# Performance work log

Measured on AMD Instinct MI355X. Metric: run time of the kernel, lower is better.

Reference implementation:

```python
import jax, jax.numpy as jnp
import numpy as np
import math

L, D, H, DH, DFF, V, NB, MAXD = 4, 512, 8, 64, 1024, 32128, 32, 128
B, S = 2, 2048
EPS = 1e-6


def gelu_new(x):
    return 0.5 * x * (1.0 + jnp.tanh(math.sqrt(2.0 / math.pi) * (x + 0.044715 * x ** 3)))


def t5_layernorm(x, w):
    var = jnp.mean(jnp.square(x.astype(jnp.float32)), axis=-1, keepdims=True)
    return w * (x * jax.lax.rsqrt(var + EPS))


def relative_position_bucket(rel_pos, num_buckets=NB, max_distance=MAXD):
    # bidirectional T5 bucketing
    nb = num_buckets // 2
    buckets = (rel_pos > 0).astype(jnp.int32) * nb
    rp = jnp.abs(rel_pos)
    max_exact = nb // 2
    is_small = rp < max_exact
    rp_large = max_exact + (
        jnp.log(jnp.maximum(rp, 1).astype(jnp.float32) / max_exact)
        / math.log(max_distance / max_exact) * (nb - max_exact)
    ).astype(jnp.int32)
    rp_large = jnp.minimum(rp_large, nb - 1)
    return buckets + jnp.where(is_small, rp, rp_large)


def compute_bias(rel_bias_table, q_len, k_len):
    ctx = jnp.arange(q_len)[:, None]
    mem = jnp.arange(k_len)[None, :]
    buckets = relative_position_bucket(mem - ctx)              # [S, S]
    vals = rel_bias_table[buckets]                             # [S, S, H]
    return jnp.transpose(vals, (2, 0, 1))[None]                # [1, H, S, S]


def setup_inputs() -> dict:
    key = jax.random.key(0)
    ks = jax.random.split(key, 12)
    s = 0.02
    return {
        "input_ids": jax.random.randint(ks[0], (B, S), 0, V),
        "embed": jax.random.normal(ks[1], (V, D), jnp.float32) * s,
        "Wq": jax.random.normal(ks[2], (L, D, H * DH), jnp.float32) * s,
        "Wk": jax.random.normal(ks[3], (L, D, H * DH), jnp.float32) * s,
        "Wv": jax.random.normal(ks[4], (L, D, H * DH), jnp.float32) * s,
        "Wo": jax.random.normal(ks[5], (L, H * DH, D), jnp.float32) * s,
        "rel_bias": jax.random.normal(ks[6], (NB, H), jnp.float32) * s,
        "wi0": jax.random.normal(ks[7], (L, D, DFF), jnp.float32) * s,
        "wi1": jax.random.normal(ks[8], (L, D, DFF), jnp.float32) * s,
        "wo_ffn": jax.random.normal(ks[9], (L, DFF, D), jnp.float32) * s,
        "ln0_w": jnp.ones((L, D), jnp.float32),
        "ln1_w": jnp.ones((L, D), jnp.float32),
        "final_ln_w": jnp.ones((D,), jnp.float32),
    }


def encoder_forward(input_ids, embed, Wq, Wk, Wv, Wo, rel_bias, wi0, wi1, wo_ffn, ln0_w, ln1_w, final_ln_w):
    x = embed[input_ids]                                       # [B, S, D]
    pos_bias = compute_bias(rel_bias, S, S)                    # [1, H, S, S], reused across layers
    for i in range(L):
        # --- self-attention (T5: no 1/sqrt(d) scaling) ---
        h = t5_layernorm(x, ln0_w[i])
        q = (h @ Wq[i]).reshape(B, S, H, DH)
        k = (h @ Wk[i]).reshape(B, S, H, DH)
        v = (h @ Wv[i]).reshape(B, S, H, DH)
        scores = jnp.einsum('bqhd,bkhd->bhqk', q, k) + pos_bias
        attn = jax.nn.softmax(scores, axis=-1)
        o = jnp.einsum('bhqk,bkhd->bqhd', attn, v).reshape(B, S, H * DH)
        x = x + o @ Wo[i]
        # --- gated-GELU FFN ---
        h = t5_layernorm(x, ln1_w[i])
        g = gelu_new(h @ wi0[i]) * (h @ wi1[i])
        x = x + g @ wo_ffn[i]
    out = t5_layernorm(x, final_ln_w)
    return out, pos_bias


def reference(input_ids, embed, Wq, Wk, Wv, Wo, rel_bias, wi0, wi1, wo_ffn, ln0_w, ln1_w, final_ln_w):
    return encoder_forward(input_ids, embed, Wq, Wk, Wv, Wo, rel_bias, wi0, wi1, wo_ffn, ln0_w, ln1_w, final_ln_w)
```

## Files before the change

### kernel.cpp

```cpp
#include <hip/hip_runtime.h>

#define NTOK 4096

typedef float f32x4 __attribute__((ext_vector_type(4)));
typedef short s16x8 __attribute__((ext_vector_type(8)));
typedef unsigned short u16x4 __attribute__((ext_vector_type(4)));
typedef unsigned short u16x8 __attribute__((ext_vector_type(8)));

__device__ __forceinline__ unsigned short fbf(float f) {
  unsigned int u = __float_as_uint(f);
  return (unsigned short)((u + 0x7FFFu + ((u >> 16) & 1u)) >> 16);
}
__device__ __forceinline__ float bf2f(unsigned short s) {
  return __uint_as_float(((unsigned int)s) << 16);
}
__device__ __forceinline__ float gelu_new_f(float x) {
  float inner = 0.7978845608028654f * (x + 0.044715f * x * x * x);
  return 0.5f * x * (1.0f + tanhf(inner));
}

__device__ __forceinline__ void gl_lds16(const void* g, void* l) {
  __builtin_amdgcn_global_load_lds(
      (const __attribute__((address_space(1))) unsigned int*)g,
      (__attribute__((address_space(3))) unsigned int*)l, 16, 0, 0);
}

__global__ void embed_kernel(const int* __restrict__ ids, const float* __restrict__ emb,
                             float* __restrict__ x) {
  int tok = blockIdx.x;
  int id = ids[tok];
  int t = threadIdx.x;
  *(float4*)(x + (size_t)tok * 512 + t * 4) = *(const float4*)(emb + (size_t)id * 512 + t * 4);
}

__global__ void build_dbias_kernel(const float* __restrict__ rel_bias, float* __restrict__ dbias) {
  int d = blockIdx.x * 256 + threadIdx.x;
  if (d >= 4096) return;
  int rel = d - 2047;
  int bucket = (rel > 0) ? 16 : 0;
  int rp = rel < 0 ? -rel : rel;
  if (rp < 8) {
    bucket += rp;
  } else {
    float v = logf((float)rp / 8.0f) / logf(16.0f) * 8.0f;
    int rl = 8 + (int)v;
    bucket += (rl < 15) ? rl : 15;
  }
  for (int hh = 0; hh < 8; ++hh)
    dbias[hh * 4096 + d] = rel_bias[bucket * 8 + hh];
}

__global__ void posbias_kernel(const float* __restrict__ dbias, float* __restrict__ out1) {
  size_t g = (size_t)blockIdx.x * 256 + threadIdx.x;
  int k4 = (int)(g & 511) * 4;
  int qq = (int)((g >> 9) & 2047);
  int hh = (int)(g >> 20);
  const float* src = dbias + hh * 4096 + (k4 - qq + 2047);
  *(float4*)(out1 + g * 4) = make_float4(src[0], src[1], src[2], src[3]);
}

__global__ void rmsnorm_bf16_kernel(const float* __restrict__ x, const float* __restrict__ w,
                                    unsigned short* __restrict__ out) {
  int tok = blockIdx.x;
  int t = threadIdx.x;
  float4 v = *(const float4*)(x + (size_t)tok * 512 + t * 4);
  float ss = v.x * v.x + v.y * v.y + v.z * v.z + v.w * v.w;
  for (int m = 1; m < 64; m <<= 1) ss += __shfl_xor(ss, m, 64);
  __shared__ float part[2];
  if ((t & 63) == 0) part[t >> 6] = ss;
  __syncthreads();
  float scale = rsqrtf((part[0] + part[1]) * (1.0f / 512.0f) + 1e-6f);
  float4 wv = *(const float4*)(w + t * 4);
  u16x4 o = {fbf(wv.x * v.x * scale), fbf(wv.y * v.y * scale),
             fbf(wv.z * v.z * scale), fbf(wv.w * v.w * scale)};
  *(u16x4*)(out + (size_t)tok * 512 + t * 4) = o;
}

__global__ void rmsnorm_f32_kernel(const float* __restrict__ x, const float* __restrict__ w,
                                   float* __restrict__ out) {
  int tok = blockIdx.x;
  int t = threadIdx.x;
  float4 v = *(const float4*)(x + (size_t)tok * 512 + t * 4);
  float ss = v.x * v.x + v.y * v.y + v.z * v.z + v.w * v.w;
  for (int m = 1; m < 64; m <<= 1) ss += __shfl_xor(ss, m, 64);
  __shared__ float part[2];
  if ((t & 63) == 0) part[t >> 6] = ss;
  __syncthreads();
  float scale = rsqrtf((part[0] + part[1]) * (1.0f / 512.0f) + 1e-6f);
  float4 wv = *(const float4*)(w + t * 4);
  *(float4*)(out + (size_t)tok * 512 + t * 4) =
      make_float4(wv.x * v.x * scale, wv.y * v.y * scale, wv.z * v.z * scale, wv.w * v.w * scale);
}

__global__ void transw_kernel(const float* S0, const float* S1, const float* S2, const float* S3,
                              unsigned short* D0, unsigned short* D1, unsigned short* D2,
                              unsigned short* D3, int R, int C) {
  __shared__ float tile[32][33];
  int mat = blockIdx.z >> 2, layer = blockIdx.z & 3;
  const float* src = (mat == 0 ? S0 : mat == 1 ? S1 : mat == 2 ? S2 : S3) + (size_t)layer * R * C;
  unsigned short* dst = (mat == 0 ? D0 : mat == 1 ? D1 : mat == 2 ? D2 : D3) + (size_t)layer * R * C;
  int t = threadIdx.x;
  int r0 = blockIdx.y * 32, c0 = blockIdx.x * 32;
  int tr = t >> 3, tc = (t & 7) * 4;
  float4 v = *(const float4*)(src + (size_t)(r0 + tr) * C + c0 + tc);
  tile[tr][tc] = v.x; tile[tr][tc + 1] = v.y; tile[tr][tc + 2] = v.z; tile[tr][tc + 3] = v.w;
  __syncthreads();
  u16x4 o = {fbf(tile[tc + 0][tr]), fbf(tile[tc + 1][tr]),
             fbf(tile[tc + 2][tr]), fbf(tile[tc + 3][tr])};
  *(u16x4*)(dst + (size_t)(c0 + tr) * R + r0 + tc) = o;
}

__global__ __launch_bounds__(256) void gemm64_kernel(
    const unsigned short* __restrict__ A,
    const unsigned short* B0, const unsigned short* B1, const unsigned short* B2,
    void* C0, void* C1, void* C2, const float* __restrict__ Res,
    int M, int N, int K, int m0, int m1, int m2) {
  __shared__ unsigned short As[2][64 * 64];
  __shared__ unsigned short Bs[2][64 * 64];
  const int z = blockIdx.z;
  const unsigned short* B = (z == 0) ? B0 : (z == 1) ? B1 : B2;
  void* Cptr = (z == 0) ? C0 : (z == 1) ? C1 : C2;
  const int mode = (z == 0) ? m0 : (z == 1) ? m1 : m2;
  const int t = threadIdx.x, lane = t & 63, w = t >> 6;
  const int quad = lane >> 4, c = lane & 15;
  const int wr = w >> 1, wc = w & 1;
  const int row0 = blockIdx.y * 64, col0 = blockIdx.x * 64;
  const int ar = t >> 3, aj = t & 7;
  const int asrc8 = (aj ^ (ar & 7)) * 8;
  const unsigned short* Agl = A + (size_t)(row0 + ar) * K + asrc8;
  const unsigned short* Bgl = B + (size_t)(col0 + ar) * K + asrc8;
  f32x4 acc[2][2];
#pragma unroll
  for (int i = 0; i < 2; ++i)
#pragma unroll
    for (int j = 0; j < 2; ++j) { f32x4 zz = {0.f, 0.f, 0.f, 0.f}; acc[i][j] = zz; }

  gl_lds16(Agl, &As[0][w * 512]);
  gl_lds16(Agl + 32 * (size_t)K, &As[0][2048 + w * 512]);
  gl_lds16(Bgl, &Bs[0][w * 512]);
  gl_lds16(Bgl + 32 * (size_t)K, &Bs[0][2048 + w * 512]);
  __syncthreads();

  int p = 0;
  for (int k0 = 0; k0 < K; k0 += 64) {
    if (k0 + 64 < K) {
      gl_lds16(Agl + k0 + 64, &As[p ^ 1][w * 512]);
      gl_lds16(Agl + k0 + 64 + 32 * (size_t)K, &As[p ^ 1][2048 + w * 512]);
      gl_lds16(Bgl + k0 + 64, &Bs[p ^ 1][w * 512]);
      gl_lds16(Bgl + k0 + 64 + 32 * (size_t)K, &Bs[p ^ 1][2048 + w * 512]);
    }
    s16x8 af[2][2], bf[2][2];
#pragma unroll
    for (int rb = 0; rb < 2; ++rb) {
      int r = wr * 32 + rb * 16 + c;
      int n = wc * 32 + rb * 16 + c;
#pragma unroll
      for (int ks = 0; ks < 2; ++ks) {
        af[rb][ks] = *(const s16x8*)&As[p][r * 64 + (((ks * 4 + quad) ^ (r & 7)) << 3)];
        bf[rb][ks] = *(const s16x8*)&Bs[p][n * 64 + (((ks * 4 + quad) ^ (n & 7)) << 3)];
      }
    }
#pragma unroll
    for (int rb = 0; rb < 2; ++rb)
#pragma unroll
      for (int cb = 0; cb < 2; ++cb)
#pragma unroll
        for (int ks = 0; ks < 2; ++ks)
          acc[rb][cb] = __builtin_amdgcn_mfma_f32_16x16x32_bf16(af[rb][ks], bf[cb][ks], acc[rb][cb], 0, 0, 0);
    __syncthreads();
    p ^= 1;
  }

  const int mb = row0 + wr * 32 + quad * 4;
  const int nb = col0 + wc * 32 + c;
  if (mode == 0) {
    unsigned short* Cp = (unsigned short*)Cptr;
#pragma unroll
    for (int rb = 0; rb < 2; ++rb)
#pragma unroll
      for (int cb = 0; cb < 2; ++cb) {
        size_t base = (size_t)(mb + rb * 16) * N + nb + cb * 16;
#pragma unroll
        for (int reg = 0; reg < 4; ++reg) Cp[base + (size_t)reg * N] = fbf(acc[rb][cb][reg]);
      }
  } else if (mode == 1) {
    unsigned short* Cp = (unsigned short*)Cptr;
#pragma unroll
    for (int rb = 0; rb < 2; ++rb)
#pragma unroll
      for (int cb = 0; cb < 2; ++cb) {
        u16x4 pk = {fbf(acc[rb][cb][0]), fbf(acc[rb][cb][1]), fbf(acc[rb][cb][2]), fbf(acc[rb][cb][3])};
        *(u16x4*)&Cp[(size_t)(nb + cb * 16) * M + mb + rb * 16] = pk;
      }
  } else {
    float* Cf = (float*)Cptr;
#pragma unroll
    for (int rb = 0; rb < 2; ++rb)
#pragma unroll
      for (int cb = 0; cb < 2; ++cb)
#pragma unroll
        for (int reg = 0; reg < 4; ++reg) {
          size_t o = (size_t)(mb + rb * 16 + reg) * N + nb + cb * 16;
          Cf[o] = Res[o] + acc[rb][cb][reg];
        }
  }
}

__global__ __launch_bounds__(256) void gemm_ffn_kernel(
    const unsigned short* __restrict__ A, const unsigned short* __restrict__ B0g,
    const unsigned short* __restrict__ B1g, unsigned short* __restrict__ C) {
  __shared__ unsigned short As[2][128 * 64];
  __shared__ unsigned short Bs0[2][64 * 64];
  __shared__ unsigned short Bs1[2][64 * 64];
  const int t = threadIdx.x, lane = t & 63, w = t >> 6;
  const int quad = lane >> 4, c = lane & 15;
  const int wr = w >> 1, wc = w & 1;
  const int row0 = blockIdx.y * 128, col0 = blockIdx.x * 64;
  const int K = 512;
  f32x4 acc0[4][2], acc1[4][2];
#pragma unroll
  for (int i = 0; i < 4; ++i)
#pragma unroll
    for (int j = 0; j < 2; ++j) {
      f32x4 zz = {0.f, 0.f, 0.f, 0.f};
      acc0[i][j] = zz; acc1[i][j] = zz;
    }

  const int ar = t >> 3, aj = t & 7;
  const int asrc8 = (aj ^ (ar & 7)) * 8;
  const unsigned short* Agl = A + (size_t)(row0 + ar) * K + asrc8;
  const unsigned short* B0gl = B0g + (size_t)(col0 + ar) * K + asrc8;
  const unsigned short* B1gl = B1g + (size_t)(col0 + ar) * K + asrc8;

  auto stage = [&](int pp, int kk) {
    gl_lds16(Agl + kk, &As[pp][w * 512]);
    gl_lds16(Agl + kk + 32 * (size_t)K, &As[pp][2048 + w * 512]);
    gl_lds16(Agl + kk + 64 * (size_t)K, &As[pp][4096 + w * 512]);
    gl_lds16(Agl + kk + 96 * (size_t)K, &As[pp][6144 + w * 512]);
    gl_lds16(B0gl + kk, &Bs0[pp][w * 512]);
    gl_lds16(B0gl + kk + 32 * (size_t)K, &Bs0[pp][2048 + w * 512]);
    gl_lds16(B1gl + kk, &Bs1[pp][w * 512]);
    gl_lds16(B1gl + kk + 32 * (size_t)K, &Bs1[pp][2048 + w * 512]);
  };

  stage(0, 0);
  __syncthreads();

  int p = 0;
  for (int k0 = 0; k0 < K; k0 += 64) {
    if (k0 + 64 < K) stage(p ^ 1, k0 + 64);
    s16x8 af[4][2], bf0[2][2], bf1[2][2];
#pragma unroll
    for (int rb = 0; rb < 4; ++rb) {
      int r = wr * 64 + rb * 16 + c;
#pragma unroll
      for (int ks = 0; ks < 2; ++ks)
        af[rb][ks] = *(const s16x8*)&As[p][r * 64 + (((ks * 4 + quad) ^ (r & 7)) << 3)];
    }
#pragma unroll
    for (int cb = 0; cb < 2; ++cb) {
      int n = wc * 32 + cb * 16 + c;
#pragma unroll
      for (int ks = 0; ks < 2; ++ks) {
        bf0[cb][ks] = *(const s16x8*)&Bs0[p][n * 64 + (((ks * 4 + quad) ^ (n & 7)) << 3)];
        bf1[cb][ks] = *(const s16x8*)&Bs1[p][n * 64 + (((ks * 4 + quad) ^ (n & 7)) << 3)];
      }
    }
#pragma unroll
    for (int rb = 0; rb < 4; ++rb)
#pragma unroll
      for (int cb = 0; cb < 2; ++cb)
#pragma unroll
        for (int ks = 0; ks < 2; ++ks) {
          acc0[rb][cb] = __builtin_amdgcn_mfma_f32_16x16x32_bf16(af[rb][ks], bf0[cb][ks], acc0[rb][cb], 0, 0, 0);
          acc1[rb][cb] = __builtin_amdgcn_mfma_f32_16x16x32_bf16(af[rb][ks], bf1[cb][ks], acc1[rb][cb], 0, 0, 0);
        }
    __syncthreads();
    p ^= 1;
  }

  const int mb = row0 + wr * 64 + quad * 4;
  const int nb = col0 + wc * 32 + c;
#pragma unroll
  for (int rb = 0; rb < 4; ++rb)
#pragma unroll
    for (int cb = 0; cb < 2; ++cb) {
      size_t base = (size_t)(mb + rb * 16) * 1024 + nb + cb * 16;
#pragma unroll
      for (int reg = 0; reg < 4; ++reg)
        C[base + (size_t)reg * 1024] = fbf(gelu_new_f(acc0[rb][cb][reg]) * acc1[rb][cb][reg]);
    }
}

__global__ __launch_bounds__(256) void attn_split_kernel(
    const unsigned short* __restrict__ qg, const unsigned short* __restrict__ kg,
    const unsigned short* __restrict__ vtg, const float* __restrict__ dbias,
    unsigned short* __restrict__ Op0, unsigned short* __restrict__ Op1,
    unsigned short* __restrict__ Op2, unsigned short* __restrict__ Op3,
    float* __restrict__ lsum) {
  __shared__ unsigned short Ks[64 * 64];
  __shared__ unsigned short Vs[64 * 64];
  __shared__ unsigned short Ps[4][16 * 64];
  __shared__ float Bb[128];
  const int b = blockIdx.z, hh = blockIdx.y;
  const int q0b = (blockIdx.x & 31) * 64;
  const int split = blockIdx.x >> 5;
  unsigned short* Op = (split == 0) ? Op0 : (split == 1) ? Op1 : (split == 2) ? Op2 : Op3;
  const int t = threadIdx.x, lane = t & 63, w = t >> 6;
  const int quad = lane >> 4, c = lane & 15;
  const int hd = hh * 64;
  s16x8 qf[2];
#pragma unroll
  for (int ks = 0; ks < 2; ++ks)
    qf[ks] = *(const s16x8*)(qg + (size_t)(b * 2048 + q0b + w * 16 + c) * 512 + hd + ks * 32 + quad * 8);
  f32x4 oacc[4];
  float psum[4];
#pragma unroll
  for (int i = 0; i < 4; ++i) {
    f32x4 zz = {0.f, 0.f, 0.f, 0.f};
    oacc[i] = zz; psum[i] = 0.f;
  }
  const int biasbase = hh * 4096 + 2047 - q0b - 63;
  const int rowloc = w * 16 + quad * 4;
  const int srow = t >> 3, sjj = t & 7;
  const unsigned short* kbase = kg + (size_t)(b * 2048) * 512 + hd;
  const unsigned short* vbase = vtg + (size_t)hd * 4096 + b * 2048;

  s16x8 kpre[2], vpre[2];
  float bpre;
  {
    int k0 = split * 8 * 64;
#pragma unroll
    for (int v = 0; v < 2; ++v) {
      int row = srow + 32 * v;
      kpre[v] = *(const s16x8*)(kbase + (size_t)(k0 + row) * 512 + sjj * 8);
      vpre[v] = *(const s16x8*)(vbase + (size_t)row * 4096 + k0 + sjj * 8);
    }
    bpre = dbias[biasbase + k0 + (t & 127)];
  }

  for (int kt = split * 8; kt < split * 8 + 8; ++kt) {
    __syncthreads();
#pragma unroll
    for (int v = 0; v < 2; ++v) {
      int row = srow + 32 * v;
      int ch = (sjj ^ (row & 7)) << 3;
      *(s16x8*)&Ks[row * 64 + ch] = kpre[v];
      *(s16x8*)&Vs[row * 64 + ch] = vpre[v];
    }
    if (t < 128) Bb[t] = bpre;
    __syncthreads();
    {
      int k0n = (kt + 1 < split * 8 + 8) ? (kt + 1) * 64 : kt * 64;
#pragma unroll
      for (int v = 0; v < 2; ++v) {
        int row = srow + 32 * v;
        kpre[v] = *(const s16x8*)(kbase + (size_t)(k0n + row) * 512 + sjj * 8);
        vpre[v] = *(const s16x8*)(vbase + (size_t)row * 4096 + k0n + sjj * 8);
      }
      bpre = dbias[biasbase + k0n + (t & 127)];
    }

    f32x4 s[4];
#pragma unroll
    for (int i = 0; i < 4; ++i) { f32x4 zz = {0.f, 0.f, 0.f, 0.f}; s[i] = zz; }
#pragma unroll
    for (int ks = 0; ks < 2; ++ks)
#pragma unroll
      for (int cb = 0; cb < 4; ++cb) {
        int n = cb * 16 + c;
        s16x8 kf = *(const s16x8*)&Ks[n * 64 + (((ks * 4 + quad) ^ (n & 7)) << 3)];
        s[cb] = __builtin_amdgcn_mfma_f32_16x16x32_bf16(qf[ks], kf, s[cb], 0, 0, 0);
      }
#pragma unroll
    for (int cb = 0; cb < 4; ++cb) {
      int col = cb * 16 + c;
      int chunkbase = (col >> 3);
#pragma unroll
      for (int reg = 0; reg < 4; ++reg) {
        float pp = __expf(s[cb][reg] + Bb[col - rowloc - reg + 63]);
        psum[reg] += pp;
        int rowp = quad * 4 + reg;
        Ps[w][rowp * 64 + ((chunkbase ^ (rowp & 7)) << 3) + (col & 7)] = fbf(pp);
      }
    }
#pragma unroll
    for (int ks = 0; ks < 2; ++ks) {
      s16x8 pf = *(const s16x8*)&Ps[w][c * 64 + (((ks * 4 + quad) ^ (c & 7)) << 3)];
#pragma unroll
      for (int cbo = 0; cbo < 4; ++cbo) {
        int n = cbo * 16 + c;
        s16x8 vf = *(const s16x8*)&Vs[n * 64 + (((ks * 4 + quad) ^ (n & 7)) << 3)];
        oacc[cbo] = __builtin_amdgcn_mfma_f32_16x16x32_bf16(pf, vf, oacc[cbo], 0, 0, 0);
      }
    }
  }
#pragma unroll
  for (int reg = 0; reg < 4; ++reg) {
    float ps = psum[reg];
    ps += __shfl_xor(ps, 1, 64);
    ps += __shfl_xor(ps, 2, 64);
    ps += __shfl_xor(ps, 4, 64);
    ps += __shfl_xor(ps, 8, 64);
    psum[reg] = ps;
  }
  const size_t obase = ((size_t)(b * 8 + hh) * 2048 + q0b + w * 16 + quad * 4);
#pragma unroll
  for (int cbo = 0; cbo < 4; ++cbo)
#pragma unroll
    for (int reg = 0; reg < 4; ++reg)
      Op[(obase + reg) * 64 + cbo * 16 + c] = fbf(oacc[cbo][reg]);
  if (c == 0) {
    const size_t lbase = (size_t)split * 32768 + (size_t)(b * 8 + hh) * 2048 + q0b + w * 16 + quad * 4;
#pragma unroll
    for (int reg = 0; reg < 4; ++reg) lsum[lbase + reg] = psum[reg];
  }
}

__global__ void attn_combine_kernel(const unsigned short* __restrict__ O0,
                                    const unsigned short* __restrict__ O1,
                                    const unsigned short* __restrict__ O2,
                                    const unsigned short* __restrict__ O3,
                                    const float* __restrict__ lsum,
                                    unsigned short* __restrict__ out) {
  int gr = blockIdx.x * 16 + (threadIdx.x >> 4);
  int d4 = (threadIdx.x & 15) * 4;
  float inv = 1.0f / (lsum[gr] + lsum[32768 + gr] + lsum[65536 + gr] + lsum[98304 + gr]);
  u16x4 p0 = *(const u16x4*)(O0 + (size_t)gr * 64 + d4);
  u16x4 p1 = *(const u16x4*)(O1 + (size_t)gr * 64 + d4);
  u16x4 p2 = *(const u16x4*)(O2 + (size_t)gr * 64 + d4);
  u16x4 p3 = *(const u16x4*)(O3 + (size_t)gr * 64 + d4);
  int bidx = gr >> 14, hidx = (gr >> 11) & 7, row = gr & 2047;
  u16x4 o;
#pragma unroll
  for (int u = 0; u < 4; ++u)
    o[u] = fbf((bf2f(p0[u]) + bf2f(p1[u]) + bf2f(p2[u]) + bf2f(p3[u])) * inv);
  *(u16x4*)(out + ((size_t)(bidx * 2048 + row) * 512) + hidx * 64 + d4) = o;
}

extern "C" void kernel_launch(void* const* d_in, const int* in_sizes, int n_in,
                              void* d_out, int out_size, void* d_ws, size_t ws_size,
                              hipStream_t stream) {
  const int*   ids      = (const int*)d_in[0];
  const float* embed    = (const float*)d_in[1];
  const float* Wq       = (const float*)d_in[2];
  const float* Wk       = (const float*)d_in[3];
  const float* Wv       = (const float*)d_in[4];
  const float* Wo       = (const float*)d_in[5];
  const float* rel_bias = (const float*)d_in[6];
  const float* wi0      = (const float*)d_in[7];
  const float* wi1      = (const float*)d_in[8];
  const float* wo_ffn   = (const float*)d_in[9];
  const float* ln0      = (const float*)d_in[10];
  const float* ln1      = (const float*)d_in[11];
  const float* final_ln = (const float*)d_in[12];
  float* out = (float*)d_out;
  char* wsb = (char*)d_ws;

  float*          x    = (float*)wsb;
  unsigned short* h    = (unsigned short*)(wsb + 8388608);
  unsigned short* qb   = (unsigned short*)(wsb + 12582912);
  unsigned short* kb   = (unsigned short*)(wsb + 16777216);
  unsigned short* vt   = (unsigned short*)(wsb + 20971520);
  unsigned short* wqT  = (unsigned short*)(wsb + 33554432);
  unsigned short* wkT  = (unsigned short*)(wsb + 35651584);
  unsigned short* wvT  = (unsigned short*)(wsb + 37748736);
  unsigned short* woT  = (unsigned short*)(wsb + 39845888);
  unsigned short* wi0T = (unsigned short*)(wsb + 41943040);
  unsigned short* wi1T = (unsigned short*)(wsb + 46137344);
  unsigned short* wofT = (unsigned short*)(wsb + 50331648);
  float*          dbias= (float*)(wsb + 54525952);
  unsigned short* t0b  = kb;
  unsigned short* Op0  = h;
  unsigned short* Op1  = (unsigned short*)(wsb + 25165824);
  unsigned short* Op2  = (unsigned short*)(wsb + 29360128);
  unsigned short* Op3  = (unsigned short*)(wsb + 56623104);
  float*          lsum = (float*)(wsb + 60817408);

  embed_kernel<<<NTOK, 128, 0, stream>>>(ids, embed, x);
  build_dbias_kernel<<<16, 256, 0, stream>>>(rel_bias, dbias);
  posbias_kernel<<<32768, 256, 0, stream>>>(dbias, out + 2097152);
  transw_kernel<<<dim3(16, 16, 16), 256, 0, stream>>>(Wq, Wk, Wv, Wo, wqT, wkT, wvT, woT, 512, 512);
  transw_kernel<<<dim3(32, 16, 8), 256, 0, stream>>>(wi0, wi1, wi0, wi0, wi0T, wi1T, wi0T, wi0T, 512, 1024);
  transw_kernel<<<dim3(16, 32, 4), 256, 0, stream>>>(wo_ffn, wo_ffn, wo_ffn, wo_ffn, wofT, wofT, wofT, wofT, 1024, 512);

  for (int l = 0; l < 4; ++l) {
    const unsigned short* wqT_l = wqT + (size_t)l * 262144;
    const unsigned short* wkT_l = wkT + (size_t)l * 262144;
    const unsigned short* wvT_l = wvT + (size_t)l * 262144;
    const unsigned short* woT_l = woT + (size_t)l * 262144;
    const unsigned short* wi0T_l = wi0T + (size_t)l * 524288;
    const unsigned short* wi1T_l = wi1T + (size_t)l * 524288;
    const unsigned short* wofT_l = wofT + (size_t)l * 524288;

    rmsnorm_bf16_kernel<<<NTOK, 128, 0, stream>>>(x, ln0 + l * 512, h);
    gemm64_kernel<<<dim3(8, 64, 3), 256, 0, stream>>>(h, wqT_l, wkT_l, wvT_l,
        qb, kb, vt, nullptr, NTOK, 512, 512, 0, 0, 1);
    attn_split_kernel<<<dim3(128, 8, 2), 256, 0, stream>>>(qb, kb, vt, dbias,
        Op0, Op1, Op2, Op3, lsum);
    attn_combine_kernel<<<2048, 256, 0, stream>>>(Op0, Op1, Op2, Op3, lsum, qb);
    gemm64_kernel<<<dim3(8, 64, 1), 256, 0, stream>>>(qb, woT_l, woT_l, woT_l,
        x, x, x, x, NTOK, 512, 512, 2, 2, 2);
    rmsnorm_bf16_kernel<<<NTOK, 128, 0, stream>>>(x, ln1 + l * 512, h);
    gemm_ffn_kernel<<<dim3(16, 32), 256, 0, stream>>>(h, wi0T_l, wi1T_l, t0b);
    gemm64_kernel<<<dim3(8, 64, 1), 256, 0, stream>>>(t0b, wofT_l, wofT_l, wofT_l,
        x, x, x, x, NTOK, 512, 1024, 2, 2, 2);
  }
  rmsnorm_f32_kernel<<<NTOK, 128, 0, stream>>>(x, final_ln, out);
}
```

Baseline: 668.9 us.

## Process 128 query rows per attention block to reuse K/V tiles

Each attention block now handles 128 query rows, 32 per wave in two 16-row sub-blocks, instead of 64. Each K/V fragment loaded from LDS feeds two MFMAs, halving LDS reads and global K/V traffic per query. The positional bias is read directly from global memory per element instead of being staged through shared memory. In exchange the grid has half as many blocks (1024), register pressure and the P scratch buffer both double, and bias loads become uncached global reads.

```diff
diff --git a/kernel.cpp b/kernel.cpp
--- a/kernel.cpp
+++ b/kernel.cpp
@@ -300,34 +300,35 @@
     float* __restrict__ lsum) {
   __shared__ unsigned short Ks[64 * 64];
   __shared__ unsigned short Vs[64 * 64];
-  __shared__ unsigned short Ps[4][16 * 64];
-  __shared__ float Bb[128];
+  __shared__ unsigned short Ps[4][32 * 64];
   const int b = blockIdx.z, hh = blockIdx.y;
-  const int q0b = (blockIdx.x & 31) * 64;
-  const int split = blockIdx.x >> 5;
+  const int q0b = (blockIdx.x & 15) * 128;
+  const int split = blockIdx.x >> 4;
   unsigned short* Op = (split == 0) ? Op0 : (split == 1) ? Op1 : (split == 2) ? Op2 : Op3;
   const int t = threadIdx.x, lane = t & 63, w = t >> 6;
   const int quad = lane >> 4, c = lane & 15;
   const int hd = hh * 64;
-  s16x8 qf[2];
-#pragma unroll
-  for (int ks = 0; ks < 2; ++ks)
-    qf[ks] = *(const s16x8*)(qg + (size_t)(b * 2048 + q0b + w * 16 + c) * 512 + hd + ks * 32 + quad * 8);
-  f32x4 oacc[4];
-  float psum[4];
-#pragma unroll
-  for (int i = 0; i < 4; ++i) {
-    f32x4 zz = {0.f, 0.f, 0.f, 0.f};
-    oacc[i] = zz; psum[i] = 0.f;
-  }
-  const int biasbase = hh * 4096 + 2047 - q0b - 63;
-  const int rowloc = w * 16 + quad * 4;
+  s16x8 qf[2][2];
+#pragma unroll
+  for (int rb = 0; rb < 2; ++rb)
+#pragma unroll
+    for (int ks = 0; ks < 2; ++ks)
+      qf[rb][ks] = *(const s16x8*)(qg + (size_t)(b * 2048 + q0b + w * 32 + rb * 16 + c) * 512 + hd + ks * 32 + quad * 8);
+  f32x4 oacc[2][4];
+  float psum[2][4];
+#pragma unroll
+  for (int rb = 0; rb < 2; ++rb)
+#pragma unroll
+    for (int i = 0; i < 4; ++i) {
+      f32x4 zz = {0.f, 0.f, 0.f, 0.f};
+      oacc[rb][i] = zz; psum[rb][i] = 0.f;
+    }
+  const float* dbl = dbias + hh * 4096 + 2047 + c - q0b - w * 32 - quad * 4;
   const int srow = t >> 3, sjj = t & 7;
   const unsigned short* kbase = kg + (size_t)(b * 2048) * 512 + hd;
   const unsigned short* vbase = vtg + (size_t)hd * 4096 + b * 2048;
 
   s16x8 kpre[2], vpre[2];
-  float bpre;
   {
     int k0 = split * 8 * 64;
 #pragma unroll
@@ -336,7 +337,6 @@
       kpre[v] = *(const s16x8*)(kbase + (size_t)(k0 + row) * 512 + sjj * 8);
       vpre[v] = *(const s16x8*)(vbase + (size_t)row * 4096 + k0 + sjj * 8);
     }
-    bpre = dbias[biasbase + k0 + (t & 127)];
   }
 
   for (int kt = split * 8; kt < split * 8 + 8; ++kt) {
@@ -348,7 +348,6 @@
       *(s16x8*)&Ks[row * 64 + ch] = kpre[v];
       *(s16x8*)&Vs[row * 64 + ch] = vpre[v];
     }
-    if (t < 128) Bb[t] = bpre;
     __syncthreads();
     {
       int k0n = (kt + 1 < split * 8 + 8) ? (kt + 1) * 64 : kt * 64;
@@ -358,62 +357,83 @@
         kpre[v] = *(const s16x8*)(kbase + (size_t)(k0n + row) * 512 + sjj * 8);
         vpre[v] = *(const s16x8*)(vbase + (size_t)row * 4096 + k0n + sjj * 8);
       }
-      bpre = dbias[biasbase + k0n + (t & 127)];
-    }
-
-    f32x4 s[4];
-#pragma unroll
-    for (int i = 0; i < 4; ++i) { f32x4 zz = {0.f, 0.f, 0.f, 0.f}; s[i] = zz; }
-#pragma unroll
-    for (int ks = 0; ks < 2; ++ks)
+    }
+
+    f32x4 s[2][4];
+#pragma unroll
+    for (int rb = 0; rb < 2; ++rb)
+#pragma unroll
+      for (int i = 0; i < 4; ++i) { f32x4 zz = {0.f, 0.f, 0.f, 0.f}; s[rb][i] = zz; }
+#pragma unroll
+    for (int cb = 0; cb < 4; ++cb) {
+      int n = cb * 16 + c;
+      s16x8 kf0 = *(const s16x8*)&Ks[n * 64 + ((quad ^ (n & 7)) << 3)];
+      s16x8 kf1 = *(const s16x8*)&Ks[n * 64 + (((4 + quad) ^ (n & 7)) << 3)];
+#pragma unroll
+      for (int rb = 0; rb < 2; ++rb) {
+        s[rb][cb] = __builtin_amdgcn_mfma_f32_16x16x32_bf16(qf[rb][0], kf0, s[rb][cb], 0, 0, 0);
+        s[rb][cb] = __builtin_amdgcn_mfma_f32_16x16x32_bf16(qf[rb][1], kf1, s[rb][cb], 0, 0, 0);
+      }
+    }
+
+    const float* dbk = dbl + kt * 64;
+#pragma unroll
+    for (int rb = 0; rb < 2; ++rb)
 #pragma unroll
       for (int cb = 0; cb < 4; ++cb) {
-        int n = cb * 16 + c;
-        s16x8 kf = *(const s16x8*)&Ks[n * 64 + (((ks * 4 + quad) ^ (n & 7)) << 3)];
-        s[cb] = __builtin_amdgcn_mfma_f32_16x16x32_bf16(qf[ks], kf, s[cb], 0, 0, 0);
-      }
-#pragma unroll
-    for (int cb = 0; cb < 4; ++cb) {
-      int col = cb * 16 + c;
-      int chunkbase = (col >> 3);
-#pragma unroll
-      for (int reg = 0; reg < 4; ++reg) {
-        float pp = __expf(s[cb][reg] + Bb[col - rowloc - reg + 63]);
-        psum[reg] += pp;
-        int rowp = quad * 4 + reg;
-        Ps[w][rowp * 64 + ((chunkbase ^ (rowp & 7)) << 3) + (col & 7)] = fbf(pp);
-      }
-    }
-#pragma unroll
-    for (int ks = 0; ks < 2; ++ks) {
-      s16x8 pf = *(const s16x8*)&Ps[w][c * 64 + (((ks * 4 + quad) ^ (c & 7)) << 3)];
-#pragma unroll
-      for (int cbo = 0; cbo < 4; ++cbo) {
-        int n = cbo * 16 + c;
-        s16x8 vf = *(const s16x8*)&Vs[n * 64 + (((ks * 4 + quad) ^ (n & 7)) << 3)];
-        oacc[cbo] = __builtin_amdgcn_mfma_f32_16x16x32_bf16(pf, vf, oacc[cbo], 0, 0, 0);
-      }
-    }
-  }
-#pragma unroll
-  for (int reg = 0; reg < 4; ++reg) {
-    float ps = psum[reg];
-    ps += __shfl_xor(ps, 1, 64);
-    ps += __shfl_xor(ps, 2, 64);
-    ps += __shfl_xor(ps, 4, 64);
-    ps += __shfl_xor(ps, 8, 64);
-    psum[reg] = ps;
-  }
-  const size_t obase = ((size_t)(b * 8 + hh) * 2048 + q0b + w * 16 + quad * 4);
-#pragma unroll
-  for (int cbo = 0; cbo < 4; ++cbo)
-#pragma unroll
-    for (int reg = 0; reg < 4; ++reg)
-      Op[(obase + reg) * 64 + cbo * 16 + c] = fbf(oacc[cbo][reg]);
-  if (c == 0) {
-    const size_t lbase = (size_t)split * 32768 + (size_t)(b * 8 + hh) * 2048 + q0b + w * 16 + quad * 4;
-#pragma unroll
-    for (int reg = 0; reg < 4; ++reg) lsum[lbase + reg] = psum[reg];
+        int col = cb * 16 + c;
+        int chunkbase = col >> 3;
+#pragma unroll
+        for (int reg = 0; reg < 4; ++reg) {
+          float pp = __expf(s[rb][cb][reg] + dbk[(cb - rb) * 16 - reg]);
+          psum[rb][reg] += pp;
+          int rowp = rb * 16 + quad * 4 + reg;
+          Ps[w][rowp * 64 + ((chunkbase ^ (rowp & 7)) << 3) + (col & 7)] = fbf(pp);
+        }
+      }
+
+    s16x8 pf[2][2];
+#pragma unroll
+    for (int rb = 0; rb < 2; ++rb)
+#pragma unroll
+      for (int ks = 0; ks < 2; ++ks)
+        pf[rb][ks] = *(const s16x8*)&Ps[w][(rb * 16 + c) * 64 + (((ks * 4 + quad) ^ (c & 7)) << 3)];
+#pragma unroll
+    for (int cbo = 0; cbo < 4; ++cbo) {
+      int n = cbo * 16 + c;
+      s16x8 vf0 = *(const s16x8*)&Vs[n * 64 + ((quad ^ (n & 7)) << 3)];
+      s16x8 vf1 = *(const s16x8*)&Vs[n * 64 + (((4 + quad) ^ (n & 7)) << 3)];
+#pragma unroll
+      for (int rb = 0; rb < 2; ++rb) {
+        oacc[rb][cbo] = __builtin_amdgcn_mfma_f32_16x16x32_bf16(pf[rb][0], vf0, oacc[rb][cbo], 0, 0, 0);
+        oacc[rb][cbo] = __builtin_amdgcn_mfma_f32_16x16x32_bf16(pf[rb][1], vf1, oacc[rb][cbo], 0, 0, 0);
+      }
+    }
+  }
+#pragma unroll
+  for (int rb = 0; rb < 2; ++rb)
+#pragma unroll
+    for (int reg = 0; reg < 4; ++reg) {
+      float ps = psum[rb][reg];
+      ps += __shfl_xor(ps, 1, 64);
+      ps += __shfl_xor(ps, 2, 64);
+      ps += __shfl_xor(ps, 4, 64);
+      ps += __shfl_xor(ps, 8, 64);
+      psum[rb][reg] = ps;
+    }
+#pragma unroll
+  for (int rb = 0; rb < 2; ++rb) {
+    const size_t obase = ((size_t)(b * 8 + hh) * 2048 + q0b + w * 32 + rb * 16 + quad * 4);
+#pragma unroll
+    for (int cbo = 0; cbo < 4; ++cbo)
+#pragma unroll
+      for (int reg = 0; reg < 4; ++reg)
+        Op[(obase + reg) * 64 + cbo * 16 + c] = fbf(oacc[rb][cbo][reg]);
+    if (c == 0) {
+      const size_t lbase = (size_t)split * 32768 + (size_t)(b * 8 + hh) * 2048 + q0b + w * 32 + rb * 16 + quad * 4;
+#pragma unroll
+      for (int reg = 0; reg < 4; ++reg) lsum[lbase + reg] = psum[rb][reg];
+    }
   }
 }
 
@@ -496,7 +516,7 @@
     rmsnorm_bf16_kernel<<<NTOK, 128, 0, stream>>>(x, ln0 + l * 512, h);
     gemm64_kernel<<<dim3(8, 64, 3), 256, 0, stream>>>(h, wqT_l, wkT_l, wvT_l,
         qb, kb, vt, nullptr, NTOK, 512, 512, 0, 0, 1);
-    attn_split_kernel<<<dim3(128, 8, 2), 256, 0, stream>>>(qb, kb, vt, dbias,
+    attn_split_kernel<<<dim3(64, 8, 2), 256, 0, stream>>>(qb, kb, vt, dbias,
         Op0, Op1, Op2, Op3, lsum);
     attn_combine_kernel<<<2048, 256, 0, stream>>>(Op0, Op1, Op2, Op3, lsum, qb);
     gemm64_kernel<<<dim3(8, 64, 1), 256, 0, stream>>>(qb, woT_l, woT_l, woT_l,
```

Measured after the change: 778.5 us. 1.16x slower.

## Enlarge GEMM row tile to 128 and double-buffer attention K/V tiles

Applied to the files above, without the earlier changes.

The generic GEMM now computes 128x64 output tiles instead of 64x64, so each wave holds 4x2 MFMA accumulators and B tiles are reused across more rows. Grids for QKV, Wo and FFN-out are halved to match. Separately, the attention kernel double-buffers K, V and bias in shared memory, which removes one of the two barriers per key tile and lets the next tile's global loads overlap compute. The cost is fewer GEMM blocks (grids of 256 or 768) on a large-CU GPU, plus more LDS and register use, which may reduce occupancy.

```diff
diff --git a/kernel.cpp b/kernel.cpp
--- a/kernel.cpp
+++ b/kernel.cpp
@@ -110,12 +110,12 @@
   *(u16x4*)(dst + (size_t)(c0 + tr) * R + r0 + tc) = o;
 }
 
-__global__ __launch_bounds__(256) void gemm64_kernel(
+__global__ __launch_bounds__(256) void gemm128_kernel(
     const unsigned short* __restrict__ A,
     const unsigned short* B0, const unsigned short* B1, const unsigned short* B2,
     void* C0, void* C1, void* C2, const float* __restrict__ Res,
     int M, int N, int K, int m0, int m1, int m2) {
-  __shared__ unsigned short As[2][64 * 64];
+  __shared__ unsigned short As[2][128 * 64];
   __shared__ unsigned short Bs[2][64 * 64];
   const int z = blockIdx.z;
   const unsigned short* B = (z == 0) ? B0 : (z == 1) ? B1 : B2;
@@ -124,44 +124,50 @@
   const int t = threadIdx.x, lane = t & 63, w = t >> 6;
   const int quad = lane >> 4, c = lane & 15;
   const int wr = w >> 1, wc = w & 1;
-  const int row0 = blockIdx.y * 64, col0 = blockIdx.x * 64;
+  const int row0 = blockIdx.y * 128, col0 = blockIdx.x * 64;
+  f32x4 acc[4][2];
+#pragma unroll
+  for (int i = 0; i < 4; ++i)
+#pragma unroll
+    for (int j = 0; j < 2; ++j) { f32x4 zz = {0.f, 0.f, 0.f, 0.f}; acc[i][j] = zz; }
+
   const int ar = t >> 3, aj = t & 7;
   const int asrc8 = (aj ^ (ar & 7)) * 8;
   const unsigned short* Agl = A + (size_t)(row0 + ar) * K + asrc8;
   const unsigned short* Bgl = B + (size_t)(col0 + ar) * K + asrc8;
-  f32x4 acc[2][2];
-#pragma unroll
-  for (int i = 0; i < 2; ++i)
-#pragma unroll
-    for (int j = 0; j < 2; ++j) { f32x4 zz = {0.f, 0.f, 0.f, 0.f}; acc[i][j] = zz; }
-
-  gl_lds16(Agl, &As[0][w * 512]);
-  gl_lds16(Agl + 32 * (size_t)K, &As[0][2048 + w * 512]);
-  gl_lds16(Bgl, &Bs[0][w * 512]);
-  gl_lds16(Bgl + 32 * (size_t)K, &Bs[0][2048 + w * 512]);
+
+  auto stage = [&](int pp, int kk) {
+    gl_lds16(Agl + kk, &As[pp][w * 512]);
+    gl_lds16(Agl + kk + 32 * (size_t)K, &As[pp][2048 + w * 512]);
+    gl_lds16(Agl + kk + 64 * (size_t)K, &As[pp][4096 + w * 512]);
+    gl_lds16(Agl + kk + 96 * (size_t)K, &As[pp][6144 + w * 512]);
+    gl_lds16(Bgl + kk, &Bs[pp][w * 512]);
+    gl_lds16(Bgl + kk + 32 * (size_t)K, &Bs[pp][2048 + w * 512]);
+  };
+
+  stage(0, 0);
   __syncthreads();
 
   int p = 0;
   for (int k0 = 0; k0 < K; k0 += 64) {
-    if (k0 + 64 < K) {
-      gl_lds16(Agl + k0 + 64, &As[p ^ 1][w * 512]);
-      gl_lds16(Agl + k0 + 64 + 32 * (size_t)K, &As[p ^ 1][2048 + w * 512]);
-      gl_lds16(Bgl + k0 + 64, &Bs[p ^ 1][w * 512]);
-      gl_lds16(Bgl + k0 + 64 + 32 * (size_t)K, &Bs[p ^ 1][2048 + w * 512]);
-    }
-    s16x8 af[2][2], bf[2][2];
-#pragma unroll
-    for (int rb = 0; rb < 2; ++rb) {
-      int r = wr * 32 + rb * 16 + c;
-      int n = wc * 32 + rb * 16 + c;
-#pragma unroll
-      for (int ks = 0; ks < 2; ++ks) {
+    if (k0 + 64 < K) stage(p ^ 1, k0 + 64);
+    s16x8 af[4][2], bf[2][2];
+#pragma unroll
+    for (int rb = 0; rb < 4; ++rb) {
+      int r = wr * 64 + rb * 16 + c;
+#pragma unroll
+      for (int ks = 0; ks < 2; ++ks)
         af[rb][ks] = *(const s16x8*)&As[p][r * 64 + (((ks * 4 + quad) ^ (r & 7)) << 3)];
-        bf[rb][ks] = *(const s16x8*)&Bs[p][n * 64 + (((ks * 4 + quad) ^ (n & 7)) << 3)];
-      }
-    }
-#pragma unroll
-    for (int rb = 0; rb < 2; ++rb)
+    }
+#pragma unroll
+    for (int cb = 0; cb < 2; ++cb) {
+      int n = wc * 32 + cb * 16 + c;
+#pragma unroll
+      for (int ks = 0; ks < 2; ++ks)
+        bf[cb][ks] = *(const s16x8*)&Bs[p][n * 64 + (((ks * 4 + quad) ^ (n & 7)) << 3)];
+    }
+#pragma unroll
+    for (int rb = 0; rb < 4; ++rb)
 #pragma unroll
       for (int cb = 0; cb < 2; ++cb)
 #pragma unroll
@@ -171,12 +177,12 @@
     p ^= 1;
   }
 
-  const int mb = row0 + wr * 32 + quad * 4;
+  const int mb = row0 + wr * 64 + quad * 4;
   const int nb = col0 + wc * 32 + c;
   if (mode == 0) {
     unsigned short* Cp = (unsigned short*)Cptr;
 #pragma unroll
-    for (int rb = 0; rb < 2; ++rb)
+    for (int rb = 0; rb < 4; ++rb)
 #pragma unroll
       for (int cb = 0; cb < 2; ++cb) {
         size_t base = (size_t)(mb + rb * 16) * N + nb + cb * 16;
@@ -186,7 +192,7 @@
   } else if (mode == 1) {
     unsigned short* Cp = (unsigned short*)Cptr;
 #pragma unroll
-    for (int rb = 0; rb < 2; ++rb)
+    for (int rb = 0; rb < 4; ++rb)
 #pragma unroll
       for (int cb = 0; cb < 2; ++cb) {
         u16x4 pk = {fbf(acc[rb][cb][0]), fbf(acc[rb][cb][1]), fbf(acc[rb][cb][2]), fbf(acc[rb][cb][3])};
@@ -195,7 +201,7 @@
   } else {
     float* Cf = (float*)Cptr;
 #pragma unroll
-    for (int rb = 0; rb < 2; ++rb)
+    for (int rb = 0; rb < 4; ++rb)
 #pragma unroll
       for (int cb = 0; cb < 2; ++cb)
 #pragma unroll
@@ -298,10 +304,10 @@
     unsigned short* __restrict__ Op0, unsigned short* __restrict__ Op1,
     unsigned short* __restrict__ Op2, unsigned short* __restrict__ Op3,
     float* __restrict__ lsum) {
-  __shared__ unsigned short Ks[64 * 64];
-  __shared__ unsigned short Vs[64 * 64];
+  __shared__ unsigned short Ks[2][64 * 64];
+  __shared__ unsigned short Vs[2][64 * 64];
   __shared__ unsigned short Ps[4][16 * 64];
-  __shared__ float Bb[128];
+  __shared__ float Bb[2][128];
   const int b = blockIdx.z, hh = blockIdx.y;
   const int q0b = (blockIdx.x & 31) * 64;
   const int split = blockIdx.x >> 5;
@@ -325,11 +331,12 @@
   const int srow = t >> 3, sjj = t & 7;
   const unsigned short* kbase = kg + (size_t)(b * 2048) * 512 + hd;
   const unsigned short* vbase = vtg + (size_t)hd * 4096 + b * 2048;
+  const int kt0 = split * 8;
 
   s16x8 kpre[2], vpre[2];
   float bpre;
-  {
-    int k0 = split * 8 * 64;
+  auto ldtile = [&](int kt) {
+    int k0 = kt * 64;
 #pragma unroll
     for (int v = 0; v < 2; ++v) {
       int row = srow + 32 * v;
@@ -337,28 +344,28 @@
       vpre[v] = *(const s16x8*)(vbase + (size_t)row * 4096 + k0 + sjj * 8);
     }
     bpre = dbias[biasbase + k0 + (t & 127)];
-  }
-
-  for (int kt = split * 8; kt < split * 8 + 8; ++kt) {
-    __syncthreads();
+  };
+  auto sttile = [&](int buf) {
 #pragma unroll
     for (int v = 0; v < 2; ++v) {
       int row = srow + 32 * v;
       int ch = (sjj ^ (row & 7)) << 3;
-      *(s16x8*)&Ks[row * 64 + ch] = kpre[v];
-      *(s16x8*)&Vs[row * 64 + ch] = vpre[v];
-    }
-    if (t < 128) Bb[t] = bpre;
-    __syncthreads();
-    {
-      int k0n = (kt + 1 < split * 8 + 8) ? (kt + 1) * 64 : kt * 64;
-#pragma unroll
-      for (int v = 0; v < 2; ++v) {
-        int row = srow + 32 * v;
-        kpre[v] = *(const s16x8*)(kbase + (size_t)(k0n + row) * 512 + sjj * 8);
-        vpre[v] = *(const s16x8*)(vbase + (size_t)row * 4096 + k0n + sjj * 8);
-      }
-      bpre = dbias[biasbase + k0n + (t & 127)];
+      *(s16x8*)&Ks[buf][row * 64 + ch] = kpre[v];
+      *(s16x8*)&Vs[buf][row * 64 + ch] = vpre[v];
+    }
+    if (t < 128) Bb[buf][t] = bpre;
+  };
+
+  ldtile(kt0);
+  sttile(0);
+  ldtile(kt0 + 1);
+  __syncthreads();
+
+  for (int kt = 0; kt < 8; ++kt) {
+    const int cur = kt & 1;
+    if (kt < 7) {
+      sttile(cur ^ 1);
+      if (kt < 6) ldtile(kt0 + kt + 2);
     }
 
     f32x4 s[4];
@@ -369,7 +376,7 @@
 #pragma unroll
       for (int cb = 0; cb < 4; ++cb) {
         int n = cb * 16 + c;
-        s16x8 kf = *(const s16x8*)&Ks[n * 64 + (((ks * 4 + quad) ^ (n & 7)) << 3)];
+        s16x8 kf = *(const s16x8*)&Ks[cur][n * 64 + (((ks * 4 + quad) ^ (n & 7)) << 3)];
         s[cb] = __builtin_amdgcn_mfma_f32_16x16x32_bf16(qf[ks], kf, s[cb], 0, 0, 0);
       }
 #pragma unroll
@@ -378,7 +385,7 @@
       int chunkbase = (col >> 3);
 #pragma unroll
       for (int reg = 0; reg < 4; ++reg) {
-        float pp = __expf(s[cb][reg] + Bb[col - rowloc - reg + 63]);
+        float pp = __expf(s[cb][reg] + Bb[cur][col - rowloc - reg + 63]);
         psum[reg] += pp;
         int rowp = quad * 4 + reg;
         Ps[w][rowp * 64 + ((chunkbase ^ (rowp & 7)) << 3) + (col & 7)] = fbf(pp);
@@ -390,10 +397,11 @@
 #pragma unroll
       for (int cbo = 0; cbo < 4; ++cbo) {
         int n = cbo * 16 + c;
-        s16x8 vf = *(const s16x8*)&Vs[n * 64 + (((ks * 4 + quad) ^ (n & 7)) << 3)];
+        s16x8 vf = *(const s16x8*)&Vs[cur][n * 64 + (((ks * 4 + quad) ^ (n & 7)) << 3)];
         oacc[cbo] = __builtin_amdgcn_mfma_f32_16x16x32_bf16(pf, vf, oacc[cbo], 0, 0, 0);
       }
     }
+    __syncthreads();
   }
 #pragma unroll
   for (int reg = 0; reg < 4; ++reg) {
@@ -494,16 +502,16 @@
     const unsigned short* wofT_l = wofT + (size_t)l * 524288;
 
     rmsnorm_bf16_kernel<<<NTOK, 128, 0, stream>>>(x, ln0 + l * 512, h);
-    gemm64_kernel<<<dim3(8, 64, 3), 256, 0, stream>>>(h, wqT_l, wkT_l, wvT_l,
+    gemm128_kernel<<<dim3(8, 32, 3), 256, 0, stream>>>(h, wqT_l, wkT_l, wvT_l,
         qb, kb, vt, nullptr, NTOK, 512, 512, 0, 0, 1);
     attn_split_kernel<<<dim3(128, 8, 2), 256, 0, stream>>>(qb, kb, vt, dbias,
         Op0, Op1, Op2, Op3, lsum);
     attn_combine_kernel<<<2048, 256, 0, stream>>>(Op0, Op1, Op2, Op3, lsum, qb);
-    gemm64_kernel<<<dim3(8, 64, 1), 256, 0, stream>>>(qb, woT_l, woT_l, woT_l,
+    gemm128_kernel<<<dim3(8, 32, 1), 256, 0, stream>>>(qb, woT_l, woT_l, woT_l,
         x, x, x, x, NTOK, 512, 512, 2, 2, 2);
     rmsnorm_bf16_kernel<<<NTOK, 128, 0, stream>>>(x, ln1 + l * 512, h);
     gemm_ffn_kernel<<<dim3(16, 32), 256, 0, stream>>>(h, wi0T_l, wi1T_l, t0b);
-    gemm64_kernel<<<dim3(8, 64, 1), 256, 0, stream>>>(t0b, wofT_l, wofT_l, wofT_l,
+    gemm128_kernel<<<dim3(8, 32, 1), 256, 0, stream>>>(t0b, wofT_l, wofT_l, wofT_l,
         x, x, x, x, NTOK, 512, 1024, 2, 2, 2);
   }
   rmsnorm_f32_kernel<<<NTOK, 128, 0, stream>>>(x, final_ln, out);
```

Measured after the change: 685.6 us. 2.5% more time.
